# Kernel optimization log

Measured on AMD Instinct MI355X. Metric: run time of the kernel, lower is better.

Reference implementation:

```python
import jax, jax.numpy as jnp
import numpy as np

B = 16384
N = 1024  # boundary vertices per row; x has 2 + 2*N columns

def setup_inputs() -> dict:
    key = jax.random.key(0)
    x = jax.random.normal(key, (B, 2 + 2 * N), dtype=jnp.float32)
    return {"x": x}

def reference(x) -> jnp.ndarray:
    # x: [B, 2+2N]; col=x[:,0], row=x[:,1], verts=x[:,2:].reshape(B,N,2)
    col = x[:, 0:1]                      # [B,1]
    row = x[:, 1:2]                      # [B,1]
    verts = x[:, 2:].reshape(x.shape[0], -1, 2)  # [B,N,2]
    # phi[i,j] = atan2(vy - row, vx - col)
    phi = jnp.arctan2(verts[:, :, 1] - row, verts[:, :, 0] - col)  # [B,N]
    # angles = phi - circular-shift-left(phi)  (torch: cat(phi[1:], phi[0]))
    angles = phi - jnp.roll(phi, -1, axis=1)
    return angles
```

## Files before the change

kernel.cpp:

```cpp
#include <hip/hip_runtime.h>


#define NVERT 1024
#define ROWSTRIDE (2 + 2 * NVERT)
#define BLK 256

__device__ __forceinline__ float fast_atan2f(float dy, float dx) {
    const float ax = __builtin_fabsf(dx);
    const float ay = __builtin_fabsf(dy);
    const float mx = fmaxf(ax, ay);
    const float mn = fminf(ax, ay);
    float t = mn * __builtin_amdgcn_rcpf(mx);
    t = (mx == 0.0f) ? 0.0f : t;
    const float s = t * t;
    float u =                  0.00282363896258175373077393f;
    u = __builtin_fmaf(u, s, -0.0159569028764963150024414f);
    u = __builtin_fmaf(u, s,  0.0425049886107444763183594f);
    u = __builtin_fmaf(u, s, -0.0748900920152664184570312f);
    u = __builtin_fmaf(u, s,  0.106347933411598205566406f);
    u = __builtin_fmaf(u, s, -0.142027363181114196777344f);
    u = __builtin_fmaf(u, s,  0.199926957488059997558594f);
    u = __builtin_fmaf(u, s, -0.333331018686294555664062f);
    float r = __builtin_fmaf(s * u, t, t);
    r = (ay > ax) ? (1.5707963267948966f - r) : r;
    r = (dx < 0.0f) ? (3.1415926535897931f - r) : r;
    return __builtin_copysignf(r, dy);
}

__global__ __launch_bounds__(BLK) void calweight_kernel(const float* __restrict__ x,
                                                        float* __restrict__ out) {
    const int b = blockIdx.x;
    const int t = threadIdx.x;

    const float* __restrict__ xr = x + (size_t)b * ROWSTRIDE;
    const float colv = xr[0];
    const float rowv = xr[1];

    __shared__ float phi[NVERT];

    const float2* __restrict__ verts = (const float2*)(xr + 2);
#pragma unroll
    for (int k = 0; k < NVERT / BLK; ++k) {
        const int j = t + k * BLK;
        const float2 v = verts[j];
        phi[j] = fast_atan2f(v.y - rowv, v.x - colv);
    }
    __syncthreads();

    float* __restrict__ orow = out + (size_t)b * NVERT;
    const int j0 = 4 * t;
    const float4 p = ((const float4*)phi)[t];
    const float pn = phi[(j0 + 4) & (NVERT - 1)];
    float4 r;
    r.x = p.x - p.y;
    r.y = p.y - p.z;
    r.z = p.z - p.w;
    r.w = p.w - pn;
    ((float4*)orow)[t] = r;
}

extern "C" void kernel_launch(void* const* d_in, const int* in_sizes, int n_in,
                              void* d_out, int out_size, void* d_ws, size_t ws_size,
                              hipStream_t stream) {
    const float* x = (const float*)d_in[0];
    float* out = (float*)d_out;
    const int B = in_sizes[0] / ROWSTRIDE;
    calweight_kernel<<<B, BLK, 0, stream>>>(x, out);
}
```

Baseline: 205.1 us.

## Process two rows per block to enable aligned float4 vertex loads

Each block now handles a pair of rows, whose combined stride is 16-byte aligned. This lets all vertex data be read with float4 loads, and a per-index decode maps each vector to its row and vertex slots. The grid is halved and each thread writes two float4 outputs. The aim is better load width and less per-block overhead, at the cost of branchy index decoding, a small tail load, and the assumption that B is even.

```diff
diff --git a/kernel.cpp b/kernel.cpp
--- a/kernel.cpp
+++ b/kernel.cpp
@@ -3,6 +3,7 @@
 
 #define NVERT 1024
 #define ROWSTRIDE (2 + 2 * NVERT)
+#define PAIRSTRIDE (2 * ROWSTRIDE)
 #define BLK 256
 
 __device__ __forceinline__ float fast_atan2f(float dy, float dx) {
@@ -29,34 +30,58 @@
 
 __global__ __launch_bounds__(BLK) void calweight_kernel(const float* __restrict__ x,
                                                         float* __restrict__ out) {
-    const int b = blockIdx.x;
+    const int pb = blockIdx.x;
     const int t = threadIdx.x;
 
-    const float* __restrict__ xr = x + (size_t)b * ROWSTRIDE;
-    const float colv = xr[0];
-    const float rowv = xr[1];
+    const float* __restrict__ xp = x + (size_t)pb * PAIRSTRIDE;
+    const float c0 = xp[0], r0 = xp[1];
+    const float c1 = xp[ROWSTRIDE], r1 = xp[ROWSTRIDE + 1];
 
-    __shared__ float phi[NVERT];
+    __shared__ float phi[2 * NVERT];
 
-    const float2* __restrict__ verts = (const float2*)(xr + 2);
+    const float4* __restrict__ vp = (const float4*)xp;
+
+    auto decode = [&](float4 v, int q) {
+        if (q == 0) {
+            phi[0] = fast_atan2f(v.w - r0, v.z - c0);
+        } else if (q < 512) {
+            const int k = 2 * q - 1;
+            phi[k]     = fast_atan2f(v.y - r0, v.x - c0);
+            phi[k + 1] = fast_atan2f(v.w - r0, v.z - c0);
+        } else if (q == 512) {
+            phi[1023] = fast_atan2f(v.y - r0, v.x - c0);
+        } else {
+            const int k = 2 * q - 2;
+            phi[k]     = fast_atan2f(v.y - r1, v.x - c1);
+            phi[k + 1] = fast_atan2f(v.w - r1, v.z - c1);
+        }
+    };
+
+    float4 v[4];
 #pragma unroll
-    for (int k = 0; k < NVERT / BLK; ++k) {
-        const int j = t + k * BLK;
-        const float2 v = verts[j];
-        phi[j] = fast_atan2f(v.y - rowv, v.x - colv);
-    }
+    for (int s = 0; s < 4; ++s) v[s] = vp[t + s * BLK];
+    float4 vt;
+    if (t == 0) vt = vp[1024];
+#pragma unroll
+    for (int s = 0; s < 4; ++s) decode(v[s], t + s * BLK);
+    if (t == 0) decode(vt, 1024);
+
     __syncthreads();
 
-    float* __restrict__ orow = out + (size_t)b * NVERT;
-    const int j0 = 4 * t;
-    const float4 p = ((const float4*)phi)[t];
-    const float pn = phi[(j0 + 4) & (NVERT - 1)];
-    float4 r;
-    r.x = p.x - p.y;
-    r.y = p.y - p.z;
-    r.z = p.z - p.w;
-    r.w = p.w - pn;
-    ((float4*)orow)[t] = r;
+    const float4* __restrict__ phi4 = (const float4*)phi;
+    const float4 p0 = phi4[t];
+    const float4 p1 = phi4[t + 256];
+    const int jn = (4 * t + 4) & (NVERT - 1);
+    const float pn0 = phi[jn];
+    const float pn1 = phi[NVERT + jn];
+
+    float4 o0, o1;
+    o0.x = p0.x - p0.y; o0.y = p0.y - p0.z; o0.z = p0.z - p0.w; o0.w = p0.w - pn0;
+    o1.x = p1.x - p1.y; o1.y = p1.y - p1.z; o1.z = p1.z - p1.w; o1.w = p1.w - pn1;
+
+    float4* __restrict__ op = (float4*)(out + (size_t)pb * (2 * NVERT));
+    op[t] = o0;
+    op[t + 256] = o1;
 }
 
 extern "C" void kernel_launch(void* const* d_in, const int* in_sizes, int n_in,
@@ -65,5 +90,5 @@
     const float* x = (const float*)d_in[0];
     float* out = (float*)d_out;
     const int B = in_sizes[0] / ROWSTRIDE;
-    calweight_kernel<<<B, BLK, 0, stream>>>(x, out);
+    calweight_kernel<<<B / 2, BLK, 0, stream>>>(x, out);
 }
```

Result: no change. 206.7 us (+0.8%).
